# Kernel tuning notes

Measured on AMD Instinct MI355X. Metric: run time of the kernel, lower is better.

The kernel has to match this reference:

```python
import jax, jax.numpy as jnp
import numpy as np

ALPHA = 0.1  # config['alpha']


def setup_inputs() -> dict:
    key = jax.random.key(0)
    k1, k2, k3, k4, k5 = jax.random.split(key, 5)
    n_bs, bit, n_cls, class_bit, n_train = 128, 48, 100, 16, 10000
    u = jax.random.normal(k1, (n_bs, bit), dtype=jnp.float32)
    # multi-hot labels (float, as in torch: y.float())
    y = jax.random.bernoulli(k2, 0.1, (n_bs, n_cls)).astype(jnp.float32)
    ind = jnp.arange(n_bs, dtype=jnp.int64)  # distinct in-range row indices
    # buffers mid-training: U holds previous class-wise codes, Y previous labels
    U = jax.random.normal(k3, (n_train, n_cls, class_bit), dtype=jnp.float32) * 0.1
    Y = jax.random.bernoulli(k4, 0.1, (n_train, n_cls)).astype(jnp.float32)
    # xavier_uniform-like init for w_D [n_class, bit, class_bit]
    limit = np.sqrt(6.0 / (bit + class_bit)).astype(np.float32)
    w_D = jax.random.uniform(k5, (n_cls, bit, class_bit), dtype=jnp.float32,
                             minval=-limit, maxval=limit)
    return {"u": u, "y": y, "ind": ind, "U": U, "Y": Y, "w_D": w_D}


def reference(u, y, ind, U, Y, w_D):
    # update label buffer: self.Y[ind, :] = y
    Y = Y.at[ind].set(y)
    # u_ = matmul(u, w_D).permute(1,0,2): [n_bs, n_cls, class_bit]
    u_ = jnp.einsum('bk,ckd->bcd', u, w_D)
    # update code buffer with detached u_ (torch: self.U[ind] = u_.data)
    U = U.at[ind].set(jax.lax.stop_gradient(u_))
    # pairwise similarity s: [n_bs, n_train, n_cls]
    s = y[:, None, :] * Y[None, :, :]
    # inner_product: sum over class_bit -> [n_bs, n_train, n_cls]
    ip = jnp.einsum('tcd,bcd->btc', U, u_)
    # stable log(1 + exp(ip)) - s*ip, exactly as the torch expression
    likelihood = (jnp.log1p(jnp.exp(-jnp.abs(ip))) + jnp.maximum(ip, 0.0)
                  - s * ip).mean()
    quantization = ALPHA * jnp.mean((u_ - jnp.sign(u_)) ** 2)
    return likelihood + quantization
```

## Files before the change

### kernel.cpp

```cpp
#include <hip/hip_runtime.h>
#include <math.h>

#define CB 16
#define ALPHA 0.1f
#define LOG2E 1.4426950408889634f
#define LN2F  0.6931471805599453f
#define MAXW 8

typedef __bf16 bf16x8 __attribute__((ext_vector_type(8)));
typedef float  f32x16 __attribute__((ext_vector_type(16)));

__device__ inline float block_reduce_256(float v, float* red) {
    #pragma unroll
    for (int off = 32; off > 0; off >>= 1) v += __shfl_down(v, off, 64);
    int lane = threadIdx.x & 63;
    int wid  = threadIdx.x >> 6;
    if (lane == 0) red[wid] = v;
    __syncthreads();
    float s = 0.f;
    if (threadIdx.x == 0) {
        int nw = blockDim.x >> 6;
        for (int w = 0; w < nw; ++w) s += red[w];
    }
    return s;
}

__global__ __launch_bounds__(256) void prep_kernel(
        const float* __restrict__ u, const float* __restrict__ y,
        const float* __restrict__ w_D,
        float* __restrict__ u_f32, __bf16* __restrict__ u_bf,
        float* __restrict__ quant_partials,
        float* __restrict__ vvec, float* __restrict__ wvec,
        int n_bs, int bit, int n_cls, int nub) {
    __shared__ float red[4];
    __shared__ float yus[4][64];
    __shared__ float sus[4][64];
    if ((int)blockIdx.x < nub) {
        int idx = blockIdx.x * 256 + threadIdx.x;
        int total = n_bs * n_cls * CB;
        float q = 0.f;
        if (idx < total) {
            int d = idx & (CB - 1);
            int c = (idx / CB) % n_cls;
            int b = idx / (CB * n_cls);
            const float* __restrict__ ur = u + (size_t)b * bit;
            const float* __restrict__ w  = w_D + (size_t)c * bit * CB + d;
            float s = 0.f;
            for (int k = 0; k < bit; ++k) s = fmaf(ur[k], w[k * CB], s);
            u_f32[idx] = s;
            u_bf[((size_t)c * n_bs + b) * CB + d] = (__bf16)(s * LOG2E);
            float sgn = (s > 0.f) ? 1.f : ((s < 0.f) ? -1.f : 0.f);
            float dd = s - sgn;
            q = dd * dd;
        }
        float bs = block_reduce_256(q, red);
        if (threadIdx.x == 0) quant_partials[blockIdx.x] = bs;
    } else {
        const int c  = blockIdx.x - nub;
        const int kk = threadIdx.x & 63;
        const int sl = threadIdx.x >> 6;
        float yv = 0.f, sv = 0.f;
        if (kk < bit) {
            const int bpp = n_bs >> 2;
            for (int b = sl * bpp; b < (sl + 1) * bpp; ++b) {
                float uv = u[(size_t)b * bit + kk];
                sv += uv;
                yv = fmaf(y[(size_t)b * n_cls + c], uv, yv);
            }
        }
        yus[sl][kk] = yv; sus[sl][kk] = sv;
        __syncthreads();
        if (sl == 0 && kk < bit) {
            yus[0][kk] = yus[0][kk] + yus[1][kk] + yus[2][kk] + yus[3][kk];
            sus[0][kk] = sus[0][kk] + sus[1][kk] + sus[2][kk] + sus[3][kk];
        }
        __syncthreads();
        if (threadIdx.x < CB) {
            const int d = threadIdx.x;
            const float* __restrict__ wdc = w_D + (size_t)c * bit * CB + d;
            float v = 0.f, w = 0.f;
            for (int k = 0; k < bit; ++k) {
                float wv = wdc[k * CB];
                v = fmaf(yus[0][k], wv, v);
                w = fmaf(sus[0][k], wv, w);
            }
            vvec[(size_t)c * CB + d] = v;
            wvec[(size_t)c * CB + d] = w;
        }
    }
}

__global__ __launch_bounds__(256, 4) void loss_main_mfma(
        const float* __restrict__ y, const float* __restrict__ U,
        const float* __restrict__ Yb, const float* __restrict__ u_f32,
        const __bf16* __restrict__ u_bf,
        const float* __restrict__ vvec, const float* __restrict__ wvec,
        const int* __restrict__ ind, float* __restrict__ partials,
        int n_bs, int n_cls, int n_train, int ntile, int GY) {
    __shared__ int pflag[MAXW * 32];
    const int tid  = threadIdx.x;
    const int lane = tid & 63;
    const int wid  = tid >> 6;
    const int c    = blockIdx.x * 4 + wid;
    const int by   = blockIdx.y;
    const int r    = lane & 31;
    const int h    = lane >> 5;
    const int nw   = (ntile - by + GY - 1) / GY;

    for (int i = tid; i < MAXW * 32; i += 256) pflag[i] = -1;
    __syncthreads();
    if (tid < n_bs) {
        int t = ind[tid];
        for (int w = 0; w < nw; ++w) {
            unsigned rl = (unsigned)(t - (by + w * GY) * 32);
            if (rl < 32u) pflag[w * 32 + rl] = tid;
        }
    }
    __syncthreads();

    const __bf16* __restrict__ ub = u_bf + (size_t)c * n_bs * CB;
    bf16x8 B[4];
    #pragma unroll
    for (int bt = 0; bt < 4; ++bt)
        B[bt] = *(const bf16x8*)(ub + (size_t)(bt * 32 + r) * CB + h * 8);
    const float* __restrict__ vp = vvec + (size_t)c * CB + h * 8;
    const float* __restrict__ wp = wvec + (size_t)c * CB + h * 8;
    float4 vp0 = *(const float4*)(vp);
    float4 vp1 = *(const float4*)(vp + 4);
    float4 wp0 = *(const float4*)(wp);
    float4 wp1 = *(const float4*)(wp + 4);

    float acc = 0.f;
    f32x16 zc = {};
    #pragma unroll 1
    for (int w = 0; w < nw; ++w) {
        const int t0  = (by + w * GY) * 32;
        const int row = t0 + r;
        const int rc  = (row < n_train) ? row : (n_train - 1);
        const float* __restrict__ ar = U + ((size_t)rc * n_cls + c) * CB + h * 8;
        float4 a0 = *(const float4*)(ar);
        float4 a1 = *(const float4*)(ar + 4);
        float Yv = Yb[(size_t)rc * n_cls + c];

        const int pf = pflag[w * 32 + r];
        if (pf >= 0) {
            const float* __restrict__ src =
                u_f32 + ((size_t)pf * n_cls + c) * CB + h * 8;
            a0 = *(const float4*)(src);
            a1 = *(const float4*)(src + 4);
            Yv = y[(size_t)pf * n_cls + c];
        }
        if (row >= n_train) {
            a0 = make_float4(0.f, 0.f, 0.f, 0.f); a1 = a0; Yv = 0.f;
        }

        float sv = a0.x*vp0.x + a0.y*vp0.y + a0.z*vp0.z + a0.w*vp0.w
                 + a1.x*vp1.x + a1.y*vp1.y + a1.z*vp1.z + a1.w*vp1.w;
        float sw = a0.x*wp0.x + a0.y*wp0.y + a0.z*wp0.z + a0.w*wp0.w
                 + a1.x*wp1.x + a1.y*wp1.y + a1.z*wp1.z + a1.w*wp1.w;

        bf16x8 A;
        A[0] = (__bf16)a0.x; A[1] = (__bf16)a0.y;
        A[2] = (__bf16)a0.z; A[3] = (__bf16)a0.w;
        A[4] = (__bf16)a1.x; A[5] = (__bf16)a1.y;
        A[6] = (__bf16)a1.z; A[7] = (__bf16)a1.w;

        float accA = 0.f;
        float pp   = 1.f;
        #pragma unroll
        for (int bt = 0; bt < 4; ++bt) {
            f32x16 D = __builtin_amdgcn_mfma_f32_32x32x16_bf16(A, B[bt], zc,
                                                               0, 0, 0);
            float a[16];
            #pragma unroll
            for (int j = 0; j < 16; ++j) {
                float ipa = fabsf(D[j]);
                a[j] = 1.0f + __builtin_amdgcn_exp2f(-ipa);
                accA += ipa;
            }
            #pragma unroll
            for (int s = 1; s < 16; s <<= 1)
                #pragma unroll
                for (int j = 0; j < 16; j += 2 * s) a[j] *= a[j + s];
            pp *= a[0];
        }
        float accL = __builtin_amdgcn_logf(pp);
        acc += LN2F * accL + (0.5f * LN2F) * accA + 0.5f * sw - Yv * sv;
    }

    #pragma unroll
    for (int off = 32; off > 0; off >>= 1)
        acc += __shfl_down(acc, off, 64);
    if (lane == 0) {
        int bid = by * gridDim.x + blockIdx.x;
        partials[bid * 4 + wid] = acc;
    }
}

__global__ __launch_bounds__(256) void finalize_kernel(
        const float* __restrict__ partials, int nblk,
        const float* __restrict__ quant_partials, int n_quant,
        float* __restrict__ out, double pad_corr,
        double like_scale, double quant_scale) {
    double s = 0.0, q = 0.0;
    for (int i = threadIdx.x; i < nblk; i += 256) s += (double)partials[i];
    for (int i = threadIdx.x; i < n_quant; i += 256) q += (double)quant_partials[i];
    #pragma unroll
    for (int off = 32; off > 0; off >>= 1) {
        s += __shfl_down(s, off, 64);
        q += __shfl_down(q, off, 64);
    }
    __shared__ double dred[4][2];
    int lane = threadIdx.x & 63, wid = threadIdx.x >> 6;
    if (lane == 0) { dred[wid][0] = s; dred[wid][1] = q; }
    __syncthreads();
    if (threadIdx.x == 0) {
        double S = dred[0][0] + dred[1][0] + dred[2][0] + dred[3][0];
        double Q = dred[0][1] + dred[1][1] + dred[2][1] + dred[3][1];
        out[0] = (float)((S - pad_corr) * like_scale + Q * quant_scale);
    }
}

extern "C" void kernel_launch(void* const* d_in, const int* in_sizes, int n_in,
                              void* d_out, int out_size, void* d_ws, size_t ws_size,
                              hipStream_t stream) {
    const float* u   = (const float*)d_in[0];
    const float* y   = (const float*)d_in[1];
    const int*   ind = (const int*)d_in[2];
    const float* U   = (const float*)d_in[3];
    const float* Yb  = (const float*)d_in[4];
    const float* w_D = (const float*)d_in[5];

    const int n_bs    = in_sizes[2];
    const int bit     = in_sizes[0] / n_bs;
    const int n_cls   = in_sizes[1] / n_bs;
    const int n_train = in_sizes[4] / n_cls;

    const int totalU = n_bs * n_cls * CB;
    const int nub    = (totalU + 255) / 256;
    const int ntile  = (n_train + 31) / 32;
    const int GY     = (ntile + MAXW - 1) / MAXW;
    const int gx     = (n_cls + 3) / 4;
    const int nblk   = GY * gx;
    const int npart  = nblk * 4;

    char* ws = (char*)d_ws;
    size_t off = 0;
    float* u_f32 = (float*)(ws + off);          off += (size_t)totalU * 4;
    __bf16* u_bf = (__bf16*)(ws + off);         off += (size_t)totalU * 2;
    off = (off + 15) & ~(size_t)15;
    float* vvec = (float*)(ws + off);           off += (size_t)n_cls * CB * 4;
    float* wvec = (float*)(ws + off);           off += (size_t)n_cls * CB * 4;
    float* quant_partials = (float*)(ws + off); off += (size_t)nub * 4;
    off = (off + 15) & ~(size_t)15;
    float* partials = (float*)(ws + off);       off += (size_t)npart * 4;

    prep_kernel<<<nub + n_cls, 256, 0, stream>>>(
        u, y, w_D, u_f32, u_bf, quant_partials, vvec, wvec,
        n_bs, bit, n_cls, nub);

    loss_main_mfma<<<dim3(gx, GY), 256, 0, stream>>>(
        y, U, Yb, u_f32, u_bf, vvec, wvec, ind, partials,
        n_bs, n_cls, n_train, ntile, GY);

    const double ln2 = 0.6931471805599453;
    const double n_pad = (double)((long long)(ntile * 32 - n_train) *
                                  (long long)n_bs * (long long)n_cls);
    const double pad_corr    = ln2 * n_pad;
    const double like_scale  = 1.0 / ((double)n_bs * n_train * n_cls);
    const double quant_scale = (double)ALPHA / (double)totalU;

    finalize_kernel<<<1, 256, 0, stream>>>(partials, npart, quant_partials, nub,
                                           (float*)d_out, pad_corr,
                                           like_scale, quant_scale);
}
```

Measured before the change: 51.67 us.

## Fuse projection prep into main MFMA loss kernel with per-block recompute

The separate prep kernel is removed. Each main-kernel block now loads u and its four classes of w_D into LDS and recomputes u_ for its classes in registers. From those it derives the bf16 MFMA B operands, the v/w reduction vectors (via cross-lane shuffles) and the quantization partials (only in the by==0 blocks). This drops one kernel launch and the global round trip of the intermediates, at the cost of redundant projection work in every blockIdx.y slice and larger LDS use that may limit occupancy. Sizes N_BS=128 and BIT=48 are now hardcoded.

```diff
diff --git a/kernel.cpp b/kernel.cpp
--- a/kernel.cpp
+++ b/kernel.cpp
@@ -6,129 +6,149 @@
 #define LOG2E 1.4426950408889634f
 #define LN2F  0.6931471805599453f
 #define MAXW 8
+#define N_BS 128
+#define BIT  48
+#define UPAD 52
 
 typedef __bf16 bf16x8 __attribute__((ext_vector_type(8)));
 typedef float  f32x16 __attribute__((ext_vector_type(16)));
 
-__device__ inline float block_reduce_256(float v, float* red) {
-    #pragma unroll
-    for (int off = 32; off > 0; off >>= 1) v += __shfl_down(v, off, 64);
-    int lane = threadIdx.x & 63;
-    int wid  = threadIdx.x >> 6;
-    if (lane == 0) red[wid] = v;
-    __syncthreads();
-    float s = 0.f;
-    if (threadIdx.x == 0) {
-        int nw = blockDim.x >> 6;
-        for (int w = 0; w < nw; ++w) s += red[w];
-    }
-    return s;
-}
-
-__global__ __launch_bounds__(256) void prep_kernel(
+__global__ __launch_bounds__(256, 4) void loss_fused(
         const float* __restrict__ u, const float* __restrict__ y,
         const float* __restrict__ w_D,
-        float* __restrict__ u_f32, __bf16* __restrict__ u_bf,
-        float* __restrict__ quant_partials,
-        float* __restrict__ vvec, float* __restrict__ wvec,
-        int n_bs, int bit, int n_cls, int nub) {
-    __shared__ float red[4];
-    __shared__ float yus[4][64];
-    __shared__ float sus[4][64];
-    if ((int)blockIdx.x < nub) {
-        int idx = blockIdx.x * 256 + threadIdx.x;
-        int total = n_bs * n_cls * CB;
-        float q = 0.f;
-        if (idx < total) {
-            int d = idx & (CB - 1);
-            int c = (idx / CB) % n_cls;
-            int b = idx / (CB * n_cls);
-            const float* __restrict__ ur = u + (size_t)b * bit;
-            const float* __restrict__ w  = w_D + (size_t)c * bit * CB + d;
-            float s = 0.f;
-            for (int k = 0; k < bit; ++k) s = fmaf(ur[k], w[k * CB], s);
-            u_f32[idx] = s;
-            u_bf[((size_t)c * n_bs + b) * CB + d] = (__bf16)(s * LOG2E);
-            float sgn = (s > 0.f) ? 1.f : ((s < 0.f) ? -1.f : 0.f);
-            float dd = s - sgn;
-            q = dd * dd;
-        }
-        float bs = block_reduce_256(q, red);
-        if (threadIdx.x == 0) quant_partials[blockIdx.x] = bs;
-    } else {
-        const int c  = blockIdx.x - nub;
-        const int kk = threadIdx.x & 63;
-        const int sl = threadIdx.x >> 6;
-        float yv = 0.f, sv = 0.f;
-        if (kk < bit) {
-            const int bpp = n_bs >> 2;
-            for (int b = sl * bpp; b < (sl + 1) * bpp; ++b) {
-                float uv = u[(size_t)b * bit + kk];
-                sv += uv;
-                yv = fmaf(y[(size_t)b * n_cls + c], uv, yv);
-            }
-        }
-        yus[sl][kk] = yv; sus[sl][kk] = sv;
-        __syncthreads();
-        if (sl == 0 && kk < bit) {
-            yus[0][kk] = yus[0][kk] + yus[1][kk] + yus[2][kk] + yus[3][kk];
-            sus[0][kk] = sus[0][kk] + sus[1][kk] + sus[2][kk] + sus[3][kk];
-        }
-        __syncthreads();
-        if (threadIdx.x < CB) {
-            const int d = threadIdx.x;
-            const float* __restrict__ wdc = w_D + (size_t)c * bit * CB + d;
-            float v = 0.f, w = 0.f;
-            for (int k = 0; k < bit; ++k) {
-                float wv = wdc[k * CB];
-                v = fmaf(yus[0][k], wv, v);
-                w = fmaf(sus[0][k], wv, w);
-            }
-            vvec[(size_t)c * CB + d] = v;
-            wvec[(size_t)c * CB + d] = w;
-        }
-    }
-}
-
-__global__ __launch_bounds__(256, 4) void loss_main_mfma(
-        const float* __restrict__ y, const float* __restrict__ U,
-        const float* __restrict__ Yb, const float* __restrict__ u_f32,
-        const __bf16* __restrict__ u_bf,
-        const float* __restrict__ vvec, const float* __restrict__ wvec,
-        const int* __restrict__ ind, float* __restrict__ partials,
-        int n_bs, int n_cls, int n_train, int ntile, int GY) {
+        const float* __restrict__ U, const float* __restrict__ Yb,
+        const int* __restrict__ ind,
+        float* __restrict__ partials, float* __restrict__ quant_partials,
+        int n_cls, int n_train, int ntile, int GY) {
+    __shared__ float smf[N_BS * UPAD + 4 * BIT * CB];
     __shared__ int pflag[MAXW * 32];
+    float* u_lds   = smf;
+    float* wd_lds  = smf + N_BS * UPAD;
+    float* u_slice = smf;
+
     const int tid  = threadIdx.x;
     const int lane = tid & 63;
     const int wid  = tid >> 6;
-    const int c    = blockIdx.x * 4 + wid;
+    const int bx   = blockIdx.x;
     const int by   = blockIdx.y;
+    const int c    = bx * 4 + wid;
     const int r    = lane & 31;
     const int h    = lane >> 5;
     const int nw   = (ntile - by + GY - 1) / GY;
 
-    for (int i = tid; i < MAXW * 32; i += 256) pflag[i] = -1;
-    __syncthreads();
-    if (tid < n_bs) {
+    pflag[tid] = -1;
+    #pragma unroll
+    for (int it = 0; it < N_BS * (BIT / 4) / 256; ++it) {
+        int f = it * 256 + tid;
+        int b = f / (BIT / 4), k4 = f % (BIT / 4);
+        *(float4*)&u_lds[b * UPAD + k4 * 4] =
+            *(const float4*)&u[(size_t)b * BIT + k4 * 4];
+    }
+    #pragma unroll
+    for (int it = 0; it < 4 * BIT * (CB / 4) / 256; ++it) {
+        int f = it * 256 + tid;
+        int cc = f / (BIT * CB / 4), rest = f % (BIT * CB / 4);
+        *(float4*)&wd_lds[cc * BIT * CB + rest * 4] =
+            *(const float4*)&w_D[(size_t)(bx * 4 + cc) * BIT * CB + rest * 4];
+    }
+    __syncthreads();
+
+    if (tid < N_BS) {
         int t = ind[tid];
         for (int w = 0; w < nw; ++w) {
             unsigned rl = (unsigned)(t - (by + w * GY) * 32);
             if (rl < 32u) pflag[w * 32 + rl] = tid;
         }
     }
-    __syncthreads();
-
-    const __bf16* __restrict__ ub = u_bf + (size_t)c * n_bs * CB;
-    bf16x8 B[4];
-    #pragma unroll
-    for (int bt = 0; bt < 4; ++bt)
-        B[bt] = *(const bf16x8*)(ub + (size_t)(bt * 32 + r) * CB + h * 8);
-    const float* __restrict__ vp = vvec + (size_t)c * CB + h * 8;
-    const float* __restrict__ wp = wvec + (size_t)c * CB + h * 8;
-    float4 vp0 = *(const float4*)(vp);
-    float4 vp1 = *(const float4*)(vp + 4);
-    float4 wp0 = *(const float4*)(wp);
-    float4 wp1 = *(const float4*)(wp + 4);
+
+    float acc0[8] = {0,0,0,0,0,0,0,0};
+    float acc1[8] = {0,0,0,0,0,0,0,0};
+    float acc2[8] = {0,0,0,0,0,0,0,0};
+    float acc3[8] = {0,0,0,0,0,0,0,0};
+    {
+        const float* __restrict__ wdc = wd_lds + wid * BIT * CB + h * 8;
+        for (int k4 = 0; k4 < BIT / 4; ++k4) {
+            float4 ub0 = *(const float4*)&u_lds[(0 * 32 + r) * UPAD + k4 * 4];
+            float4 ub1 = *(const float4*)&u_lds[(1 * 32 + r) * UPAD + k4 * 4];
+            float4 ub2 = *(const float4*)&u_lds[(2 * 32 + r) * UPAD + k4 * 4];
+            float4 ub3 = *(const float4*)&u_lds[(3 * 32 + r) * UPAD + k4 * 4];
+            #pragma unroll
+            for (int kk = 0; kk < 4; ++kk) {
+                const float* wrow = wdc + (k4 * 4 + kk) * CB;
+                float w8[8];
+                float4 wa = *(const float4*)(wrow);
+                float4 wb = *(const float4*)(wrow + 4);
+                w8[0]=wa.x; w8[1]=wa.y; w8[2]=wa.z; w8[3]=wa.w;
+                w8[4]=wb.x; w8[5]=wb.y; w8[6]=wb.z; w8[7]=wb.w;
+                float s0 = (&ub0.x)[kk], s1 = (&ub1.x)[kk];
+                float s2 = (&ub2.x)[kk], s3 = (&ub3.x)[kk];
+                #pragma unroll
+                for (int j = 0; j < 8; ++j) {
+                    acc0[j] = fmaf(s0, w8[j], acc0[j]);
+                    acc1[j] = fmaf(s1, w8[j], acc1[j]);
+                    acc2[j] = fmaf(s2, w8[j], acc2[j]);
+                    acc3[j] = fmaf(s3, w8[j], acc3[j]);
+                }
+            }
+        }
+    }
+
+    if (by == 0) {
+        float q = 0.f;
+        #pragma unroll
+        for (int j = 0; j < 8; ++j) {
+            float v, sgn, d;
+            v = acc0[j]; sgn = (v>0.f)?1.f:((v<0.f)?-1.f:0.f); d = v-sgn; q = fmaf(d,d,q);
+            v = acc1[j]; sgn = (v>0.f)?1.f:((v<0.f)?-1.f:0.f); d = v-sgn; q = fmaf(d,d,q);
+            v = acc2[j]; sgn = (v>0.f)?1.f:((v<0.f)?-1.f:0.f); d = v-sgn; q = fmaf(d,d,q);
+            v = acc3[j]; sgn = (v>0.f)?1.f:((v<0.f)?-1.f:0.f); d = v-sgn; q = fmaf(d,d,q);
+        }
+        #pragma unroll
+        for (int off = 32; off > 0; off >>= 1) q += __shfl_down(q, off, 64);
+        if (lane == 0) quant_partials[bx * 4 + wid] = q;
+    }
+
+    float ypc0 = y[(size_t)(0 * 32 + r) * n_cls + c];
+    float ypc1 = y[(size_t)(1 * 32 + r) * n_cls + c];
+    float ypc2 = y[(size_t)(2 * 32 + r) * n_cls + c];
+    float ypc3 = y[(size_t)(3 * 32 + r) * n_cls + c];
+    float vv[8], ww[8];
+    #pragma unroll
+    for (int j = 0; j < 8; ++j) {
+        ww[j] = acc0[j] + acc1[j] + acc2[j] + acc3[j];
+        vv[j] = ypc0*acc0[j] + ypc1*acc1[j] + ypc2*acc2[j] + ypc3*acc3[j];
+    }
+    #pragma unroll
+    for (int m = 1; m < 32; m <<= 1) {
+        #pragma unroll
+        for (int j = 0; j < 8; ++j) {
+            vv[j] += __shfl_xor(vv[j], m, 64);
+            ww[j] += __shfl_xor(ww[j], m, 64);
+        }
+    }
+
+    bf16x8 B0, B1, B2, B3;
+    #pragma unroll
+    for (int j = 0; j < 8; ++j) {
+        B0[j] = (__bf16)(acc0[j] * LOG2E);
+        B1[j] = (__bf16)(acc1[j] * LOG2E);
+        B2[j] = (__bf16)(acc2[j] * LOG2E);
+        B3[j] = (__bf16)(acc3[j] * LOG2E);
+    }
+
+    __syncthreads();
+    {
+        float* dst = u_slice + wid * N_BS * CB + r * CB + h * 8;
+        *(float4*)(dst + 0*32*CB)     = make_float4(acc0[0],acc0[1],acc0[2],acc0[3]);
+        *(float4*)(dst + 0*32*CB + 4) = make_float4(acc0[4],acc0[5],acc0[6],acc0[7]);
+        *(float4*)(dst + 1*32*CB)     = make_float4(acc1[0],acc1[1],acc1[2],acc1[3]);
+        *(float4*)(dst + 1*32*CB + 4) = make_float4(acc1[4],acc1[5],acc1[6],acc1[7]);
+        *(float4*)(dst + 2*32*CB)     = make_float4(acc2[0],acc2[1],acc2[2],acc2[3]);
+        *(float4*)(dst + 2*32*CB + 4) = make_float4(acc2[4],acc2[5],acc2[6],acc2[7]);
+        *(float4*)(dst + 3*32*CB)     = make_float4(acc3[0],acc3[1],acc3[2],acc3[3]);
+        *(float4*)(dst + 3*32*CB + 4) = make_float4(acc3[4],acc3[5],acc3[6],acc3[7]);
+    }
+    __syncthreads();
 
     float acc = 0.f;
     f32x16 zc = {};
@@ -144,8 +164,7 @@
 
         const int pf = pflag[w * 32 + r];
         if (pf >= 0) {
-            const float* __restrict__ src =
-                u_f32 + ((size_t)pf * n_cls + c) * CB + h * 8;
+            const float* src = u_slice + wid * N_BS * CB + pf * CB + h * 8;
             a0 = *(const float4*)(src);
             a1 = *(const float4*)(src + 4);
             Yv = y[(size_t)pf * n_cls + c];
@@ -154,10 +173,10 @@
             a0 = make_float4(0.f, 0.f, 0.f, 0.f); a1 = a0; Yv = 0.f;
         }
 
-        float sv = a0.x*vp0.x + a0.y*vp0.y + a0.z*vp0.z + a0.w*vp0.w
-                 + a1.x*vp1.x + a1.y*vp1.y + a1.z*vp1.z + a1.w*vp1.w;
-        float sw = a0.x*wp0.x + a0.y*wp0.y + a0.z*wp0.z + a0.w*wp0.w
-                 + a1.x*wp1.x + a1.y*wp1.y + a1.z*wp1.z + a1.w*wp1.w;
+        float sv = a0.x*vv[0] + a0.y*vv[1] + a0.z*vv[2] + a0.w*vv[3]
+                 + a1.x*vv[4] + a1.y*vv[5] + a1.z*vv[6] + a1.w*vv[7];
+        float sw = a0.x*ww[0] + a0.y*ww[1] + a0.z*ww[2] + a0.w*ww[3]
+                 + a1.x*ww[4] + a1.y*ww[5] + a1.z*ww[6] + a1.w*ww[7];
 
         bf16x8 A;
         A[0] = (__bf16)a0.x; A[1] = (__bf16)a0.y;
@@ -169,7 +188,8 @@
         float pp   = 1.f;
         #pragma unroll
         for (int bt = 0; bt < 4; ++bt) {
-            f32x16 D = __builtin_amdgcn_mfma_f32_32x32x16_bf16(A, B[bt], zc,
+            bf16x8 Bf = (bt == 0) ? B0 : (bt == 1) ? B1 : (bt == 2) ? B2 : B3;
+            f32x16 D = __builtin_amdgcn_mfma_f32_32x32x16_bf16(A, Bf, zc,
                                                                0, 0, 0);
             float a[16];
             #pragma unroll
@@ -192,7 +212,7 @@
     for (int off = 32; off > 0; off >>= 1)
         acc += __shfl_down(acc, off, 64);
     if (lane == 0) {
-        int bid = by * gridDim.x + blockIdx.x;
+        int bid = by * gridDim.x + bx;
         partials[bid * 4 + wid] = acc;
     }
 }
@@ -232,36 +252,25 @@
     const float* w_D = (const float*)d_in[5];
 
     const int n_bs    = in_sizes[2];
-    const int bit     = in_sizes[0] / n_bs;
     const int n_cls   = in_sizes[1] / n_bs;
     const int n_train = in_sizes[4] / n_cls;
 
     const int totalU = n_bs * n_cls * CB;
-    const int nub    = (totalU + 255) / 256;
     const int ntile  = (n_train + 31) / 32;
     const int GY     = (ntile + MAXW - 1) / MAXW;
     const int gx     = (n_cls + 3) / 4;
     const int nblk   = GY * gx;
     const int npart  = nblk * 4;
+    const int nquant = gx * 4;
 
     char* ws = (char*)d_ws;
     size_t off = 0;
-    float* u_f32 = (float*)(ws + off);          off += (size_t)totalU * 4;
-    __bf16* u_bf = (__bf16*)(ws + off);         off += (size_t)totalU * 2;
-    off = (off + 15) & ~(size_t)15;
-    float* vvec = (float*)(ws + off);           off += (size_t)n_cls * CB * 4;
-    float* wvec = (float*)(ws + off);           off += (size_t)n_cls * CB * 4;
-    float* quant_partials = (float*)(ws + off); off += (size_t)nub * 4;
-    off = (off + 15) & ~(size_t)15;
-    float* partials = (float*)(ws + off);       off += (size_t)npart * 4;
-
-    prep_kernel<<<nub + n_cls, 256, 0, stream>>>(
-        u, y, w_D, u_f32, u_bf, quant_partials, vvec, wvec,
-        n_bs, bit, n_cls, nub);
-
-    loss_main_mfma<<<dim3(gx, GY), 256, 0, stream>>>(
-        y, U, Yb, u_f32, u_bf, vvec, wvec, ind, partials,
-        n_bs, n_cls, n_train, ntile, GY);
+    float* partials = (float*)(ws + off);        off += (size_t)npart * 4;
+    float* quant_partials = (float*)(ws + off);  off += (size_t)nquant * 4;
+
+    loss_fused<<<dim3(gx, GY), 256, 0, stream>>>(
+        u, y, w_D, U, Yb, ind, partials, quant_partials,
+        n_cls, n_train, ntile, GY);
 
     const double ln2 = 0.6931471805599453;
     const double n_pad = (double)((long long)(ntile * 32 - n_train) *
@@ -270,7 +279,8 @@
     const double like_scale  = 1.0 / ((double)n_bs * n_train * n_cls);
     const double quant_scale = (double)ALPHA / (double)totalU;
 
-    finalize_kernel<<<1, 256, 0, stream>>>(partials, npart, quant_partials, nub,
+    finalize_kernel<<<1, 256, 0, stream>>>(partials, npart,
+                                           quant_partials, nquant,
                                            (float*)d_out, pad_corr,
                                            like_scale, quant_scale);
 }
```

Result: faster. 49.41 us (-4.4%).
